# Optimization experiments

Measured on AMD Instinct MI355X. Metric: run time of the kernel, lower is better.

## Reference

```python
import jax, jax.numpy as jnp
import numpy as np

D = 64          # hidden_dim
S = 16          # neighbor_samples
BS = 1024       # batch size
K = 10          # top-k candidates for self-attention
N_ENT = 200001  # item_num + 1 (padding row)
N_EDGE = 1000000
N_REL = 64
N_USER = 50001
AGG = 1.0       # agg_param


def setup_inputs() -> dict:
    key = jax.random.key(0)
    ks = jax.random.split(key, 24)
    rn = lambda k, s: jax.random.normal(k, s, dtype=jnp.float32) * 0.05
    inp = {}
    inp["relations"] = jax.random.randint(ks[0], (BS,), 0, N_REL)
    inp["entity_pairs"] = jax.random.randint(ks[1], (BS, 2), 0, N_ENT - 1)
    inp["train_edges"] = jax.random.randint(ks[2], (BS,), 0, N_EDGE)
    inp["user_ids"] = jax.random.randint(ks[3], (BS,), 0, N_USER - 1)
    inp["top_k_ids"] = jax.random.randint(ks[4], (BS, K), 0, N_ENT - 1)
    inp["entity2edges"] = jax.random.randint(ks[5], (N_ENT, S), 0, N_EDGE)
    inp["edge2entities"] = jax.random.randint(ks[6], (N_EDGE, 2), 0, N_ENT - 1)
    inp["edge2relation"] = jax.random.randint(ks[7], (N_EDGE,), 0, N_REL)
    inp["ent_emb"] = rn(ks[8], (N_ENT, D))
    inp["rel_emb"] = rn(ks[9], (N_REL, D))
    inp["user_emb"] = rn(ks[10], (N_USER, D))
    # ConcatAggregator weights, stored [in, out] (torch Linear is x @ W.T + b)
    inp["w_ent0"] = rn(ks[11], (2 * D, D)); inp["b_ent0"] = jnp.zeros((D,), jnp.float32)
    inp["w0"] = rn(ks[12], (3 * D, D));     inp["b0"] = jnp.zeros((D,), jnp.float32)
    inp["w_ent1"] = rn(ks[13], (2 * D, D)); inp["b_ent1"] = jnp.zeros((D,), jnp.float32)
    inp["w1"] = rn(ks[14], (3 * D, D));     inp["b1"] = jnp.zeros((D,), jnp.float32)
    # SelfAttention q/k/v
    inp["wq"] = rn(ks[15], (D, D)); inp["bq"] = jnp.zeros((D,), jnp.float32)
    inp["wk"] = rn(ks[16], (D, D)); inp["bk"] = jnp.zeros((D,), jnp.float32)
    inp["wv"] = rn(ks[17], (D, D)); inp["bv"] = jnp.zeros((D,), jnp.float32)
    # mlp scorer
    inp["w_s"] = rn(ks[18], (D, 1)); inp["b_s"] = jnp.zeros((1,), jnp.float32)
    return inp


def _concat_aggregate(self_v, nb_ent, nb_edge, masks, w_ent, b_ent, w, b):
    """Aggregator.forward (masked mean over neighbor samples) + ConcatAggregator._call.
    self_v:  [bs, n, D]       edge self vectors
    nb_ent:  [bs, n, 2, D]    endpoint entity vectors
    nb_edge: [bs, n, 2, S, D] neighbor edge vectors
    masks:   [bs, n, 2, S, 1]
    """
    nei = jnp.sum(masks, axis=-2)                       # [bs,n,2,1]
    nei = jnp.where(nei == 0.0, 1.0, nei)
    edge_mean = jnp.sum(nb_edge * masks, axis=-2) / nei  # [bs,n,2,D]
    nv = jnp.concatenate([nb_ent, AGG * edge_mean], axis=-1) @ w_ent + b_ent  # [bs,n,2,D]
    bs = self_v.shape[0]
    nv2 = nv.reshape(bs, -1, 2 * D)                     # fold entity-pair dim into features
    sv = jnp.concatenate([self_v.reshape(bs, -1, D), AGG * nv2], axis=-1) @ w + b
    return sv                                            # [bs,n,D]


def reference(relations, entity_pairs, train_edges, user_ids, top_k_ids,
              entity2edges, edge2entities, edge2relation,
              ent_emb, rel_emb, user_emb,
              w_ent0, b_ent0, w0, b0, w_ent1, b_ent1, w1, b1,
              wq, bq, wk, bk, wv, bv, w_s, b_s):
    bs = relations.shape[0]
    # ---- _get_entity_neighbors_and_masks (train mode, 2 hops) ----
    edges0 = entity2edges[entity_pairs].reshape(bs, 2 * S)          # [bs,2S]
    mask0 = (edges0 != train_edges[:, None]).astype(jnp.float32).reshape(bs, 1, 2, S, 1)
    nodes1 = edge2entities[edges0]                                  # [bs,2S,2]
    edges1 = entity2edges[nodes1].reshape(bs, 2 * S * 2 * S)        # [bs,2S*2*S]
    mask1 = (edges1 != train_edges[:, None]).astype(jnp.float32).reshape(bs, 2 * S, 2, S, 1)
    # edge (relation) vectors per hop
    ev0 = rel_emb[relations][:, None, :]                            # [bs,1,D]
    ev1 = rel_emb[edge2relation[edges0]]                            # [bs,2S,D]
    ev2 = rel_emb[edge2relation[edges1]]                            # [bs,2S*2*S,D]
    # entity vectors per hop
    en0 = ent_emb[entity_pairs].reshape(bs, 1, 2, D)
    en1 = ent_emb[nodes1]                                           # [bs,2S,2,D]
    # ---- iterative aggregation (aggregators[i] shared across remaining hops) ----
    v0 = _concat_aggregate(ev0, en0, ev1.reshape(bs, 1, 2, S, D), mask0, w_ent0, b_ent0, w0, b0)
    v1 = _concat_aggregate(ev1, en1, ev2.reshape(bs, 2 * S, 2, S, D), mask1, w_ent0, b_ent0, w0, b0)
    v0 = _concat_aggregate(v0, en0, v1.reshape(bs, 1, 2, S, D), mask0, w_ent1, b_ent1, w1, b1)
    ctx = v0.reshape(bs, D)                                         # context embedding
    # ---- SelfAttention over top-k candidate embeddings ----
    u = user_emb[user_ids]                                          # [bs,D]
    tk = ent_emb[top_k_ids]                                         # [bs,K,D]
    q = (u @ wq + bq)[:, None, :]                                   # [bs,1,D]
    k_ = tk @ wk + bk                                               # [bs,K,D]
    v_ = tk @ wv + bv
    att = jax.nn.softmax(jnp.einsum('bqd,bkd->bqk', q, k_) / (float(D) ** 0.5), axis=-1)
    u_att = jnp.einsum('bqk,bkd->bqd', att, v_)[:, 0]               # [bs,D]
    # ---- final score: attended-user x context dot + mlp scorer ----
    score = jnp.sum(u_att * ctx, axis=-1) + (ctx @ w_s + b_s)[:, 0]
    return score
```

## Files before the change

### kernel.cpp

```cpp
#include <hip/hip_runtime.h>
#include <hip/hip_fp16.h>
#include <math.h>

#define DEV static __device__ __forceinline__

typedef float f32x4 __attribute__((ext_vector_type(4)));
typedef _Float16 f16x8 __attribute__((ext_vector_type(8)));

DEV _Float16 f2h(float x) { return (_Float16)x; }

DEV f16x8 ld_cvt8(const float* __restrict__ p) {
  const float4 a = *(const float4*)p;
  const float4 b = *(const float4*)(p + 4);
  f16x8 r;
  r[0] = f2h(a.x); r[1] = f2h(a.y); r[2] = f2h(a.z); r[3] = f2h(a.w);
  r[4] = f2h(b.x); r[5] = f2h(b.y); r[6] = f2h(b.z); r[7] = f2h(b.w);
  return r;
}

DEV float wave_sum64(float v) {
  v += __shfl_xor(v, 32, 64);
  v += __shfl_xor(v, 16, 64);
  v += __shfl_xor(v, 8, 64);
  v += __shfl_xor(v, 4, 64);
  v += __shfl_xor(v, 2, 64);
  v += __shfl_xor(v, 1, 64);
  return v;
}

DEV int frag_off(int k, int n) {
  const int kc = k >> 5, lg2 = (k >> 3) & 3, jj = k & 7;
  const int nt = n >> 4, ln = lg2 * 16 + (n & 15);
  return ((kc * 4 + nt) * 64 + ln) * 8 + jj;
}

__global__ __launch_bounds__(512)
void k_front(const int* __restrict__ relations, const int* __restrict__ entity_pairs,
             const int* __restrict__ train_edges,
             const int* __restrict__ entity2edges, const int* __restrict__ edge2entities,
             const int* __restrict__ edge2relation,
             const float* __restrict__ rel_emb, const float* __restrict__ w_ent0,
             const float* __restrict__ w0, const float* __restrict__ w_ent1,
             const float* __restrict__ w1,
             const int* __restrict__ user_ids, const int* __restrict__ top_k_ids,
             const float* __restrict__ user_emb, const float* __restrict__ ent_emb,
             const float* __restrict__ wq, const float* __restrict__ bq,
             const float* __restrict__ wk, const float* __restrict__ bk,
             const float* __restrict__ wv, const float* __restrict__ bv,
             _Float16* __restrict__ Xacc, int* __restrict__ idx,
             int* __restrict__ rsel_arr,
             _Float16* __restrict__ B1frag, _Float16* __restrict__ w0frag,
             _Float16* __restrict__ wefrag, _Float16* __restrict__ w1frag,
             float* __restrict__ qout, _Float16* __restrict__ kkb,
             _Float16* __restrict__ vvb, int bs, int npack, int natt)
{
  __shared__ __align__(16) unsigned char smem[24576];
  const int lane = threadIdx.x & 63;
  const int wid = threadIdx.x >> 6;

  if ((int)blockIdx.x < npack) {
    const int w = blockIdx.x * 8 + wid;
    const int b = w >> 2;
    const int q = w & 3;
    if (b >= bs) return;

    const int te = __builtin_amdgcn_readfirstlane(train_edges[b]);
    const int n0p = __builtin_amdgcn_readfirstlane(entity_pairs[b * 2 + 0]);
    const int n1p = __builtin_amdgcn_readfirstlane(entity_pairs[b * 2 + 1]);

    const int l5 = lane & 31;
    const int ent0 = (l5 >> 4) ? n1p : n0p;
    const int e0 = entity2edges[ent0 * 16 + (l5 & 15)];
    const int r0 = edge2relation[e0];

    const int itemBase = b * 33;

    int na0[4], na1[4], nb0[4], nb1[4];
#pragma unroll
    for (int t = 0; t < 4; ++t) {
      const int j0 = q * 8 + 2 * t;
      const int ea = __builtin_amdgcn_readlane(e0, j0);
      const int eb = __builtin_amdgcn_readlane(e0, j0 + 1);
      na0[t] = __builtin_amdgcn_readfirstlane(edge2entities[ea * 2 + 0]);
      na1[t] = __builtin_amdgcn_readfirstlane(edge2entities[ea * 2 + 1]);
      nb0[t] = __builtin_amdgcn_readfirstlane(edge2entities[eb * 2 + 0]);
      nb1[t] = __builtin_amdgcn_readfirstlane(edge2entities[eb * 2 + 1]);
    }
    int e_[4];
#pragma unroll
    for (int t = 0; t < 4; ++t) {
      const int ent = (lane < 16) ? na0[t] : (lane < 32) ? na1[t]
                    : (lane < 48) ? nb0[t] : nb1[t];
      e_[t] = entity2edges[ent * 16 + (lane & 15)];
    }
    unsigned long long bal_[4];
    int r_[4];
#pragma unroll
    for (int t = 0; t < 4; ++t) {
      const bool keep = (e_[t] != te);
      bal_[t] = __ballot(keep);
      const int rr = edge2relation[e_[t]];
      r_[t] = keep ? rr : 64;
    }
#pragma unroll
    for (int t = 0; t < 4; ++t) {
      int ha0 = 0, ha1 = 0, hb0 = 0, hb1 = 0;
#pragma unroll
      for (int s = 0; s < 16; ++s) {
        ha0 += (__builtin_amdgcn_readlane(r_[t], s) == lane) ? 1 : 0;
        ha1 += (__builtin_amdgcn_readlane(r_[t], s + 16) == lane) ? 1 : 0;
        hb0 += (__builtin_amdgcn_readlane(r_[t], s + 32) == lane) ? 1 : 0;
        hb1 += (__builtin_amdgcn_readlane(r_[t], s + 48) == lane) ? 1 : 0;
      }
      const int ca0 = __popcll(bal_[t] & 0xFFFFull);
      const int ca1 = __popcll(bal_[t] & 0xFFFF0000ull);
      const int cb0 = __popcll(bal_[t] & 0xFFFF00000000ull);
      const int cb1 = __popcll(bal_[t] >> 48);
      const int j0 = q * 8 + 2 * t;
      const int it0 = itemBase + j0, it1 = it0 + 1;
      Xacc[(size_t)(2 * it0 + 0) * 64 + lane] = f2h((float)ha0 / (float)(ca0 ? ca0 : 1));
      Xacc[(size_t)(2 * it0 + 1) * 64 + lane] = f2h((float)ha1 / (float)(ca1 ? ca1 : 1));
      Xacc[(size_t)(2 * it1 + 0) * 64 + lane] = f2h((float)hb0 / (float)(cb0 ? cb0 : 1));
      Xacc[(size_t)(2 * it1 + 1) * 64 + lane] = f2h((float)hb1 / (float)(cb1 ? cb1 : 1));
      if (lane == 0) {
        idx[2 * it0 + 0] = na0[t]; idx[2 * it0 + 1] = na1[t];
        idx[2 * it1 + 0] = nb0[t]; idx[2 * it1 + 1] = nb1[t];
        rsel_arr[it0] = __builtin_amdgcn_readlane(r0, j0);
        rsel_arr[it1] = __builtin_amdgcn_readlane(r0, j0 + 1);
      }
    }
    if (q == 3) {
      const int it = itemBase + 32;
      const bool keep0 = (e0 != te);
      const unsigned long long bal0 = __ballot(keep0);
      const int r0m = keep0 ? r0 : 64;
      int h0 = 0, h1 = 0;
#pragma unroll
      for (int s = 0; s < 16; ++s) {
        h0 += (__builtin_amdgcn_readlane(r0m, s) == lane) ? 1 : 0;
        h1 += (__builtin_amdgcn_readlane(r0m, s + 16) == lane) ? 1 : 0;
      }
      const int c0 = __popcll(bal0 & 0xFFFFull);
      const int c1 = __popcll(bal0 & 0xFFFF0000ull);
      Xacc[(size_t)(2 * it + 0) * 64 + lane] = f2h((float)h0 / (float)(c0 ? c0 : 1));
      Xacc[(size_t)(2 * it + 1) * 64 + lane] = f2h((float)h1 / (float)(c1 ? c1 : 1));
      if (lane == 0) {
        idx[2 * it + 0] = n0p;
        idx[2 * it + 1] = n1p;
        rsel_arr[it] = relations[b];
      }
    }
    return;
  }

  if ((int)blockIdx.x < npack + natt) {
    _Float16* Bq = (_Float16*)smem;
    _Float16* Bk = Bq + 4096;
    _Float16* Bv = Bq + 8192;
    for (int t = threadIdx.x; t < 4096; t += 512) {
      const int k = t >> 6, n = t & 63;
      const int off = frag_off(k, n);
      Bq[off] = f2h(wq[t]); Bk[off] = f2h(wk[t]); Bv[off] = f2h(wv[t]);
    }
    __syncthreads();

    const int row0 = (((int)blockIdx.x - npack) * 8 + wid) * 16;
    if (row0 >= bs * 11) return;
    const int l15 = lane & 15, lg = lane >> 4;

    if (row0 < bs) {
      const int uid = user_ids[row0 + l15];
      float bs4[4];
#pragma unroll
      for (int nt = 0; nt < 4; ++nt) bs4[nt] = bq[nt * 16 + l15];
      f32x4 acc[4];
#pragma unroll
      for (int nt = 0; nt < 4; ++nt) acc[nt] = (f32x4)(0.f);
#pragma unroll
      for (int kc = 0; kc < 2; ++kc) {
        const f16x8 A = ld_cvt8(user_emb + (size_t)uid * 64 + kc * 32 + lg * 8);
#pragma unroll
        for (int nt = 0; nt < 4; ++nt) {
          const f16x8 Bf = *(const f16x8*)&Bq[((kc * 4 + nt) * 64 + lane) * 8];
          acc[nt] = __builtin_amdgcn_mfma_f32_16x16x32_f16(A, Bf, acc[nt], 0, 0, 0);
        }
      }
#pragma unroll
      for (int nt = 0; nt < 4; ++nt)
#pragma unroll
        for (int r = 0; r < 4; ++r)
          qout[(size_t)(row0 + lg * 4 + r) * 64 + nt * 16 + l15] = acc[nt][r] + bs4[nt];
    } else {
      const int r2 = row0 - bs + l15;
      const int tid = top_k_ids[r2];
      float bsk[4], bsv[4];
#pragma unroll
      for (int nt = 0; nt < 4; ++nt) { bsk[nt] = bk[nt * 16 + l15]; bsv[nt] = bv[nt * 16 + l15]; }
      f32x4 ak[4], av[4];
#pragma unroll
      for (int nt = 0; nt < 4; ++nt) { ak[nt] = (f32x4)(0.f); av[nt] = (f32x4)(0.f); }
#pragma unroll
      for (int kc = 0; kc < 2; ++kc) {
        const f16x8 A = ld_cvt8(ent_emb + (size_t)tid * 64 + kc * 32 + lg * 8);
#pragma unroll
        for (int nt = 0; nt < 4; ++nt) {
          const f16x8 Bfk = *(const f16x8*)&Bk[((kc * 4 + nt) * 64 + lane) * 8];
          const f16x8 Bfv = *(const f16x8*)&Bv[((kc * 4 + nt) * 64 + lane) * 8];
          ak[nt] = __builtin_amdgcn_mfma_f32_16x16x32_f16(A, Bfk, ak[nt], 0, 0, 0);
          av[nt] = __builtin_amdgcn_mfma_f32_16x16x32_f16(A, Bfv, av[nt], 0, 0, 0);
        }
      }
#pragma unroll
      for (int nt = 0; nt < 4; ++nt) {
#pragma unroll
        for (int r = 0; r < 4; ++r) {
          const int rr = row0 - bs + lg * 4 + r;
          kkb[(size_t)rr * 64 + nt * 16 + l15] = f2h(ak[nt][r] + bsk[nt]);
          vvb[(size_t)rr * 64 + nt * 16 + l15] = f2h(av[nt][r] + bsv[nt]);
        }
      }
    }
    return;
  }

  {
    const int local = (int)blockIdx.x - npack - natt;
    if (local < 8) {
      for (int e = local * 512 + threadIdx.x; e < 8192; e += 8 * 512) {
        const int k = e >> 6, n = e & 63;
        float v;
        if (k < 64) {
          v = w_ent0[k * 64 + n];
        } else {
          const int m = k - 64;
          v = 0.f;
#pragma unroll 8
          for (int kk = 0; kk < 64; ++kk)
            v = fmaf(rel_emb[m * 64 + kk], w_ent0[(64 + kk) * 64 + n], v);
        }
        B1frag[frag_off(k, n)] = f2h(v);
      }
    } else {
      const int l2 = local - 8;
      for (int e = l2 * 512 + threadIdx.x; e < 32768; e += 8 * 512) {
        if (e < 12288) {
          w0frag[frag_off(e >> 6, e & 63)] = f2h(w0[e]);
        } else if (e < 20480) {
          const int t = e - 12288;
          wefrag[frag_off(t >> 6, t & 63)] = f2h(w_ent1[t]);
        } else {
          const int t = e - 20480;
          w1frag[frag_off(t >> 6, t & 63)] = f2h(w1[t]);
        }
      }
    }
  }
}

__global__ __launch_bounds__(256)
void k_mid(const _Float16* __restrict__ Xacc, const int* __restrict__ idx,
           const int* __restrict__ rsel_arr,
           const float* __restrict__ ent_emb, const float* __restrict__ rel_emb,
           const _Float16* __restrict__ B1frag, const _Float16* __restrict__ w0frag,
           const float* __restrict__ b_ent0, const float* __restrict__ b0,
           float* __restrict__ v1, int n_items)
{
  __shared__ _Float16 Lrel[64 * 64];
  __shared__ __align__(16) _Float16 nvl[4][32][72];

  for (int t = threadIdx.x; t < 4096; t += 256) Lrel[t] = f2h(rel_emb[t]);
  __syncthreads();

  const int lane = threadIdx.x & 63;
  const int wid = threadIdx.x >> 6;
  const int i0 = (blockIdx.x * 4 + wid) * 16;
  if (i0 >= n_items) return;
  const int row0 = i0 * 2;
  const int l15 = lane & 15, lg = lane >> 4;

  {
    const int e0 = idx[row0 + l15];
    const int e1 = idx[row0 + 16 + l15];
    float bs4[4];
#pragma unroll
    for (int nt = 0; nt < 4; ++nt) bs4[nt] = b_ent0[nt * 16 + l15];

    f32x4 acc0[4], acc1[4];
#pragma unroll
    for (int nt = 0; nt < 4; ++nt) { acc0[nt] = (f32x4)(0.f); acc1[nt] = (f32x4)(0.f); }

#pragma unroll
    for (int kc = 0; kc < 2; ++kc) {
      const f16x8 A0 = ld_cvt8(ent_emb + (size_t)e0 * 64 + kc * 32 + lg * 8);
      const f16x8 A1 = ld_cvt8(ent_emb + (size_t)e1 * 64 + kc * 32 + lg * 8);
#pragma unroll
      for (int nt = 0; nt < 4; ++nt) {
        const f16x8 Bf = *(const f16x8*)&B1frag[((kc * 4 + nt) * 64 + lane) * 8];
        acc0[nt] = __builtin_amdgcn_mfma_f32_16x16x32_f16(A0, Bf, acc0[nt], 0, 0, 0);
        acc1[nt] = __builtin_amdgcn_mfma_f32_16x16x32_f16(A1, Bf, acc1[nt], 0, 0, 0);
      }
    }
    const _Float16* x0 = Xacc + (size_t)(row0 + l15) * 64 + lg * 8;
    const _Float16* x1 = Xacc + (size_t)(row0 + 16 + l15) * 64 + lg * 8;
#pragma unroll
    for (int kc2 = 0; kc2 < 2; ++kc2) {
      const f16x8 A0 = *(const f16x8*)(x0 + kc2 * 32);
      const f16x8 A1 = *(const f16x8*)(x1 + kc2 * 32);
#pragma unroll
      for (int nt = 0; nt < 4; ++nt) {
        const f16x8 Bf = *(const f16x8*)&B1frag[(((kc2 + 2) * 4 + nt) * 64 + lane) * 8];
        acc0[nt] = __builtin_amdgcn_mfma_f32_16x16x32_f16(A0, Bf, acc0[nt], 0, 0, 0);
        acc1[nt] = __builtin_amdgcn_mfma_f32_16x16x32_f16(A1, Bf, acc1[nt], 0, 0, 0);
      }
    }

#pragma unroll
    for (int mt = 0; mt < 2; ++mt) {
#pragma unroll
      for (int nt = 0; nt < 4; ++nt) {
#pragma unroll
        for (int r = 0; r < 4; ++r) {
          const int lr = mt * 16 + lg * 4 + r;
          const float v = (mt ? acc1[nt][r] : acc0[nt][r]) + bs4[nt];
          nvl[wid][lr][nt * 16 + l15] = f2h(v);
        }
      }
    }
  }

  {
    const int rs = rsel_arr[i0 + l15];
    float bs4[4];
#pragma unroll
    for (int nt = 0; nt < 4; ++nt) bs4[nt] = b0[nt * 16 + l15];

    f32x4 acc[4];
#pragma unroll
    for (int nt = 0; nt < 4; ++nt) acc[nt] = (f32x4)(0.f);

#pragma unroll
    for (int kc = 0; kc < 6; ++kc) {
      f16x8 A;
      if (kc < 2) A = *(const f16x8*)&Lrel[rs * 64 + kc * 32 + lg * 8];
      else if (kc < 4) A = *(const f16x8*)&nvl[wid][2 * l15][(kc - 2) * 32 + lg * 8];
      else A = *(const f16x8*)&nvl[wid][2 * l15 + 1][(kc - 4) * 32 + lg * 8];
#pragma unroll
      for (int nt = 0; nt < 4; ++nt) {
        const f16x8 Bf = *(const f16x8*)&w0frag[((kc * 4 + nt) * 64 + lane) * 8];
        acc[nt] = __builtin_amdgcn_mfma_f32_16x16x32_f16(A, Bf, acc[nt], 0, 0, 0);
      }
    }

#pragma unroll
    for (int nt = 0; nt < 4; ++nt) {
#pragma unroll
      for (int r = 0; r < 4; ++r) {
        const int item = i0 + lg * 4 + r;
        v1[(size_t)item * 64 + nt * 16 + l15] = acc[nt][r] + bs4[nt];
      }
    }
  }
}

__global__ __launch_bounds__(256)
void k_hop2(const int* __restrict__ entity_pairs, const int* __restrict__ train_edges,
            const int* __restrict__ entity2edges, const float* __restrict__ v1,
            const float* __restrict__ ent_emb,
            const _Float16* __restrict__ wefrag, const float* __restrict__ b_ent1,
            const _Float16* __restrict__ w1frag, const float* __restrict__ b1,
            const float* __restrict__ qbuf, const _Float16* __restrict__ kkb,
            const _Float16* __restrict__ vvb,
            const float* __restrict__ w_s, const float* __restrict__ b_s,
            float* __restrict__ out, int bs)
{
  __shared__ __align__(16) _Float16 Xl[8][64];
  __shared__ __align__(16) _Float16 nvl[8][64];
  __shared__ float ctxl[4][64];

  const int lane = threadIdx.x & 63;
  const int wid = threadIdx.x >> 6;
  const int b0 = blockIdx.x * 4;
  const int myb = b0 + wid;
  const int l15 = lane & 15, lg = lane >> 4;

  if (myb < bs) {
    const int te = __builtin_amdgcn_readfirstlane(train_edges[myb]);
    const int n0 = __builtin_amdgcn_readfirstlane(entity_pairs[myb * 2 + 0]);
    const int n1 = __builtin_amdgcn_readfirstlane(entity_pairs[myb * 2 + 1]);
    const int myent = ((lane >> 4) & 1) ? n1 : n0;
    const int e = entity2edges[myent * 16 + (lane & 15)];
    const unsigned long long bal = __ballot(e != te);
    const int c0 = __popcll(bal & 0xFFFFull);
    const int c1 = __popcll(bal & 0xFFFF0000ull);
    const float* vbase = v1 + (size_t)myb * 33 * 64;
    float a0 = 0.f, a1 = 0.f;
#pragma unroll
    for (int s = 0; s < 16; ++s) {
      const float mA = (float)((bal >> s) & 1ull);
      const float mB = (float)((bal >> (s + 16)) & 1ull);
      a0 = fmaf(mA, vbase[s * 64 + lane], a0);
      a1 = fmaf(mB, vbase[(16 + s) * 64 + lane], a1);
    }
    Xl[wid * 2 + 0][lane] = f2h(a0 / (float)(c0 ? c0 : 1));
    Xl[wid * 2 + 1][lane] = f2h(a1 / (float)(c1 ? c1 : 1));
  }
  __syncthreads();

  if (wid == 0) {
    const int mm = l15 & 7;
    const int bm = min(b0 + (mm >> 1), bs - 1);
    const int side = mm & 1;
    const int ent = entity_pairs[bm * 2 + side];
    float bs4[4];
#pragma unroll
    for (int nt = 0; nt < 4; ++nt) bs4[nt] = b_ent1[nt * 16 + l15];
    f32x4 acc[4];
#pragma unroll
    for (int nt = 0; nt < 4; ++nt) acc[nt] = (f32x4)(0.f);
#pragma unroll
    for (int kc = 0; kc < 2; ++kc) {
      const f16x8 A = ld_cvt8(ent_emb + (size_t)ent * 64 + kc * 32 + lg * 8);
#pragma unroll
      for (int nt = 0; nt < 4; ++nt) {
        const f16x8 Bf = *(const f16x8*)&wefrag[((kc * 4 + nt) * 64 + lane) * 8];
        acc[nt] = __builtin_amdgcn_mfma_f32_16x16x32_f16(A, Bf, acc[nt], 0, 0, 0);
      }
    }
#pragma unroll
    for (int kc2 = 0; kc2 < 2; ++kc2) {
      const f16x8 A = *(const f16x8*)&Xl[mm][kc2 * 32 + lg * 8];
#pragma unroll
      for (int nt = 0; nt < 4; ++nt) {
        const f16x8 Bf = *(const f16x8*)&wefrag[(((kc2 + 2) * 4 + nt) * 64 + lane) * 8];
        acc[nt] = __builtin_amdgcn_mfma_f32_16x16x32_f16(A, Bf, acc[nt], 0, 0, 0);
      }
    }
#pragma unroll
    for (int nt = 0; nt < 4; ++nt) {
#pragma unroll
      for (int r = 0; r < 4; ++r) {
        const int m = lg * 4 + r;
        if (m < 8) nvl[m][nt * 16 + l15] = f2h(acc[nt][r] + bs4[nt]);
      }
    }
  }
  __syncthreads();

  if (wid == 0) {
    const int mb = min(b0 + (l15 & 3), bs - 1);
    float bs4[4];
#pragma unroll
    for (int nt = 0; nt < 4; ++nt) bs4[nt] = b1[nt * 16 + l15];
    f32x4 acc[4];
#pragma unroll
    for (int nt = 0; nt < 4; ++nt) acc[nt] = (f32x4)(0.f);
    const float* selfp = v1 + ((size_t)mb * 33 + 32) * 64;
#pragma unroll
    for (int kc = 0; kc < 6; ++kc) {
      f16x8 A;
      if (kc < 2) A = ld_cvt8(selfp + kc * 32 + lg * 8);
      else A = *(const f16x8*)&nvl[2 * (l15 & 3) + (kc >= 4 ? 1 : 0)][(kc & 1) * 32 + lg * 8];
#pragma unroll
      for (int nt = 0; nt < 4; ++nt) {
        const f16x8 Bf = *(const f16x8*)&w1frag[((kc * 4 + nt) * 64 + lane) * 8];
        acc[nt] = __builtin_amdgcn_mfma_f32_16x16x32_f16(A, Bf, acc[nt], 0, 0, 0);
      }
    }
#pragma unroll
    for (int nt = 0; nt < 4; ++nt) {
#pragma unroll
      for (int r = 0; r < 4; ++r) {
        const int m = lg * 4 + r;
        if (m < 4) ctxl[m][nt * 16 + l15] = acc[nt][r] + bs4[nt];
      }
    }
  }
  __syncthreads();

  if (myb >= bs) return;
  const float q = qbuf[(size_t)myb * 64 + lane];
  const float ctx = ctxl[wid][lane];
  float lgt[10], vvl[10];
#pragma unroll
  for (int k = 0; k < 10; ++k) {
    const float kk = (float)kkb[(size_t)(myb * 10 + k) * 64 + lane];
    vvl[k] = (float)vvb[(size_t)(myb * 10 + k) * 64 + lane];
    lgt[k] = wave_sum64(q * kk) * 0.125f;
  }
  float m = lgt[0];
#pragma unroll
  for (int k = 1; k < 10; ++k) m = fmaxf(m, lgt[k]);
  float den = 0.f;
  float att[10];
#pragma unroll
  for (int k = 0; k < 10; ++k) { att[k] = expf(lgt[k] - m); den += att[k]; }
  const float invden = 1.0f / den;
  float uatt = 0.f;
#pragma unroll
  for (int k = 0; k < 10; ++k) uatt = fmaf(att[k] * invden, vvl[k], uatt);

  const float sc = wave_sum64(uatt * ctx + ctx * w_s[lane]);
  if (lane == 0) out[myb] = sc + b_s[0];
}

extern "C" void kernel_launch(void* const* d_in, const int* in_sizes, int n_in,
                              void* d_out, int out_size, void* d_ws, size_t ws_size,
                              hipStream_t stream) {
  const int* relations     = (const int*)d_in[0];
  const int* entity_pairs  = (const int*)d_in[1];
  const int* train_edges   = (const int*)d_in[2];
  const int* user_ids      = (const int*)d_in[3];
  const int* top_k_ids     = (const int*)d_in[4];
  const int* entity2edges  = (const int*)d_in[5];
  const int* edge2entities = (const int*)d_in[6];
  const int* edge2relation = (const int*)d_in[7];
  const float* ent_emb  = (const float*)d_in[8];
  const float* rel_emb  = (const float*)d_in[9];
  const float* user_emb = (const float*)d_in[10];
  const float* w_ent0 = (const float*)d_in[11];
  const float* b_ent0 = (const float*)d_in[12];
  const float* w0     = (const float*)d_in[13];
  const float* b0     = (const float*)d_in[14];
  const float* w_ent1 = (const float*)d_in[15];
  const float* b_ent1 = (const float*)d_in[16];
  const float* w1     = (const float*)d_in[17];
  const float* b1     = (const float*)d_in[18];
  const float* wq  = (const float*)d_in[19];
  const float* bq  = (const float*)d_in[20];
  const float* wk  = (const float*)d_in[21];
  const float* bk  = (const float*)d_in[22];
  const float* wv  = (const float*)d_in[23];
  const float* bv  = (const float*)d_in[24];
  const float* w_s = (const float*)d_in[25];
  const float* b_s = (const float*)d_in[26];

  const int bs = in_sizes[0];
  const int n_items = bs * 33;
  const int rows1 = 2 * n_items;

  char* p = (char*)d_ws;
  float* v1 = (float*)p;            p += (size_t)n_items * 64 * 4;
  float* qbuf = (float*)p;          p += (size_t)bs * 64 * 4;
  _Float16* Xacc1 = (_Float16*)p;   p += (size_t)rows1 * 64 * 2;
  _Float16* kkb = (_Float16*)p;     p += (size_t)bs * 10 * 64 * 2;
  _Float16* vvb = (_Float16*)p;     p += (size_t)bs * 10 * 64 * 2;
  _Float16* B1frag = (_Float16*)p;  p += 8192 * 2;
  _Float16* w0frag = (_Float16*)p;  p += 12288 * 2;
  _Float16* wefrag = (_Float16*)p;  p += 8192 * 2;
  _Float16* w1frag = (_Float16*)p;  p += 12288 * 2;
  int* idx1 = (int*)p;              p += (size_t)rows1 * 4;
  int* rselA = (int*)p;

  const int npack = (bs * 4 + 7) / 8;
  const int natt = (bs * 11 + 127) / 128;
  const int nfront = npack + natt + 16;

  k_front<<<dim3(nfront), dim3(512), 0, stream>>>(
      relations, entity_pairs, train_edges, entity2edges, edge2entities,
      edge2relation, rel_emb, w_ent0, w0, w_ent1, w1,
      user_ids, top_k_ids, user_emb, ent_emb,
      wq, bq, wk, bk, wv, bv, Xacc1, idx1, rselA,
      B1frag, w0frag, wefrag, w1frag, qbuf, kkb, vvb,
      bs, npack, natt);

  k_mid<<<dim3((n_items + 63) / 64), dim3(256), 0, stream>>>(
      Xacc1, idx1, rselA, ent_emb, rel_emb, B1frag, w0frag,
      b_ent0, b0, v1, n_items);

  k_hop2<<<dim3((bs + 3) / 4), dim3(256), 0, stream>>>(
      entity_pairs, train_edges, entity2edges, v1, ent_emb,
      wefrag, b_ent1, w1frag, b1, qbuf, kkb, vvb, w_s, b_s,
      (float*)d_out, bs);
}
```

Baseline: 43.82 us.

## Halve per-wave items in k_mid and drop shared rel_emb staging

Each wave in k_mid now handles 8 items instead of 16, so the grid doubles in size. The first GEMM runs one 16-row MFMA tile instead of two, and the second GEMM computes 16 rows but keeps only 8, with half the lanes skipping the store. The per-block staging of the whole rel_emb table into LDS and its barrier are removed; relation rows are read from global memory and converted on the fly. This aims to raise parallelism and cut block startup cost, at the price of redundant MFMA work and more scattered global reads.

```diff
diff --git a/kernel.cpp b/kernel.cpp
--- a/kernel.cpp
+++ b/kernel.cpp
@@ -265,71 +265,58 @@
            const float* __restrict__ b_ent0, const float* __restrict__ b0,
            float* __restrict__ v1, int n_items)
 {
-  __shared__ _Float16 Lrel[64 * 64];
-  __shared__ __align__(16) _Float16 nvl[4][32][72];
-
-  for (int t = threadIdx.x; t < 4096; t += 256) Lrel[t] = f2h(rel_emb[t]);
-  __syncthreads();
+  __shared__ __align__(16) _Float16 nvl[4][16][72];
 
   const int lane = threadIdx.x & 63;
   const int wid = threadIdx.x >> 6;
-  const int i0 = (blockIdx.x * 4 + wid) * 16;
+  const int i0 = (blockIdx.x * 4 + wid) * 8;
   if (i0 >= n_items) return;
   const int row0 = i0 * 2;
   const int l15 = lane & 15, lg = lane >> 4;
 
   {
     const int e0 = idx[row0 + l15];
-    const int e1 = idx[row0 + 16 + l15];
     float bs4[4];
 #pragma unroll
     for (int nt = 0; nt < 4; ++nt) bs4[nt] = b_ent0[nt * 16 + l15];
 
-    f32x4 acc0[4], acc1[4];
-#pragma unroll
-    for (int nt = 0; nt < 4; ++nt) { acc0[nt] = (f32x4)(0.f); acc1[nt] = (f32x4)(0.f); }
+    f32x4 acc0[4];
+#pragma unroll
+    for (int nt = 0; nt < 4; ++nt) acc0[nt] = (f32x4)(0.f);
 
 #pragma unroll
     for (int kc = 0; kc < 2; ++kc) {
       const f16x8 A0 = ld_cvt8(ent_emb + (size_t)e0 * 64 + kc * 32 + lg * 8);
-      const f16x8 A1 = ld_cvt8(ent_emb + (size_t)e1 * 64 + kc * 32 + lg * 8);
 #pragma unroll
       for (int nt = 0; nt < 4; ++nt) {
         const f16x8 Bf = *(const f16x8*)&B1frag[((kc * 4 + nt) * 64 + lane) * 8];
         acc0[nt] = __builtin_amdgcn_mfma_f32_16x16x32_f16(A0, Bf, acc0[nt], 0, 0, 0);
-        acc1[nt] = __builtin_amdgcn_mfma_f32_16x16x32_f16(A1, Bf, acc1[nt], 0, 0, 0);
       }
     }
     const _Float16* x0 = Xacc + (size_t)(row0 + l15) * 64 + lg * 8;
-    const _Float16* x1 = Xacc + (size_t)(row0 + 16 + l15) * 64 + lg * 8;
 #pragma unroll
     for (int kc2 = 0; kc2 < 2; ++kc2) {
       const f16x8 A0 = *(const f16x8*)(x0 + kc2 * 32);
-      const f16x8 A1 = *(const f16x8*)(x1 + kc2 * 32);
 #pragma unroll
       for (int nt = 0; nt < 4; ++nt) {
         const f16x8 Bf = *(const f16x8*)&B1frag[(((kc2 + 2) * 4 + nt) * 64 + lane) * 8];
         acc0[nt] = __builtin_amdgcn_mfma_f32_16x16x32_f16(A0, Bf, acc0[nt], 0, 0, 0);
-        acc1[nt] = __builtin_amdgcn_mfma_f32_16x16x32_f16(A1, Bf, acc1[nt], 0, 0, 0);
-      }
-    }
-
-#pragma unroll
-    for (int mt = 0; mt < 2; ++mt) {
-#pragma unroll
-      for (int nt = 0; nt < 4; ++nt) {
-#pragma unroll
-        for (int r = 0; r < 4; ++r) {
-          const int lr = mt * 16 + lg * 4 + r;
-          const float v = (mt ? acc1[nt][r] : acc0[nt][r]) + bs4[nt];
-          nvl[wid][lr][nt * 16 + l15] = f2h(v);
-        }
+      }
+    }
+
+#pragma unroll
+    for (int nt = 0; nt < 4; ++nt) {
+#pragma unroll
+      for (int r = 0; r < 4; ++r) {
+        const int lr = lg * 4 + r;
+        nvl[wid][lr][nt * 16 + l15] = f2h(acc0[nt][r] + bs4[nt]);
       }
     }
   }
 
   {
-    const int rs = rsel_arr[i0 + l15];
+    const int l15m = l15 & 7;
+    const int rs = rsel_arr[i0 + l15m];
     float bs4[4];
 #pragma unroll
     for (int nt = 0; nt < 4; ++nt) bs4[nt] = b0[nt * 16 + l15];
@@ -341,9 +328,9 @@
 #pragma unroll
     for (int kc = 0; kc < 6; ++kc) {
       f16x8 A;
-      if (kc < 2) A = *(const f16x8*)&Lrel[rs * 64 + kc * 32 + lg * 8];
-      else if (kc < 4) A = *(const f16x8*)&nvl[wid][2 * l15][(kc - 2) * 32 + lg * 8];
-      else A = *(const f16x8*)&nvl[wid][2 * l15 + 1][(kc - 4) * 32 + lg * 8];
+      if (kc < 2) A = ld_cvt8(rel_emb + (size_t)rs * 64 + kc * 32 + lg * 8);
+      else if (kc < 4) A = *(const f16x8*)&nvl[wid][2 * l15m][(kc - 2) * 32 + lg * 8];
+      else A = *(const f16x8*)&nvl[wid][2 * l15m + 1][(kc - 4) * 32 + lg * 8];
 #pragma unroll
       for (int nt = 0; nt < 4; ++nt) {
         const f16x8 Bf = *(const f16x8*)&w0frag[((kc * 4 + nt) * 64 + lane) * 8];
@@ -351,12 +338,14 @@
       }
     }
 
-#pragma unroll
-    for (int nt = 0; nt < 4; ++nt) {
-#pragma unroll
-      for (int r = 0; r < 4; ++r) {
-        const int item = i0 + lg * 4 + r;
-        v1[(size_t)item * 64 + nt * 16 + l15] = acc[nt][r] + bs4[nt];
+    if (lg < 2) {
+#pragma unroll
+      for (int nt = 0; nt < 4; ++nt) {
+#pragma unroll
+        for (int r = 0; r < 4; ++r) {
+          const int item = i0 + lg * 4 + r;
+          v1[(size_t)item * 64 + nt * 16 + l15] = acc[nt][r] + bs4[nt];
+        }
       }
     }
   }
@@ -563,7 +552,7 @@
       B1frag, w0frag, wefrag, w1frag, qbuf, kkb, vvb,
       bs, npack, natt);
 
-  k_mid<<<dim3((n_items + 63) / 64), dim3(256), 0, stream>>>(
+  k_mid<<<dim3((n_items / 8 + 3) / 4), dim3(256), 0, stream>>>(
       Xacc1, idx1, rselA, ent_emb, rel_emb, B1frag, w0frag,
       b_ent0, b0, v1, n_items);
 
```

Result: slower. 47.37 us (+8.1%).
